# Optimization experiments

Hardware: AMD Instinct MI355X
Metric: run time of the kernel (lower is better)

## Reference

```python
import jax, jax.numpy as jnp
import numpy as np

PATCH_WEIGHT = 0.5  # module init kwarg
B, C, H = 2, 4, 128  # vol dims (H=W=D)
N, P = 128, 32       # num patches total, patch edge (Hp=Wp=Dp)


def setup_inputs() -> dict:
    key = jax.random.key(0)
    k1, k2, k3 = jax.random.split(key, 3)
    patches = jax.random.normal(k1, (N, C, P, P, P), dtype=jnp.float32)
    vol = jax.random.normal(k2, (B, C, H, H, H), dtype=jnp.float32)
    # lower bound in [0, H-P] so the PxPxP slice stays in-bounds; center = lower + P//2
    crop_centers = jax.random.randint(k3, (N, 3), 0, H - P + 1, dtype=jnp.int32) + P // 2
    return {"patches": patches, "vol": vol, "crop_centers": crop_centers}


def reference(patches, vol, crop_centers):
    n, c_dim, p = patches.shape[0], patches.shape[1], patches.shape[2]
    b_dim = vol.shape[0]
    num_patch_per_batch = n // b_dim
    b_idx = jnp.arange(n) // num_patch_per_batch            # [N] batch index per patch
    lo = crop_centers - p // 2                              # [N,3] slice lower bounds
    offs = jnp.arange(p)
    hi = lo[:, 0, None] + offs                              # [N,P]
    wi = lo[:, 1, None] + offs                              # [N,P]
    di = lo[:, 2, None] + offs                              # [N,P]
    c_idx = jnp.arange(c_dim)
    # module: new_vol = vol*(1-pw); w_t is overwritten with ones, so add pw*patch
    new_vol = vol * (1.0 - PATCH_WEIGHT)
    new_vol = new_vol.at[
        b_idx[:, None, None, None, None],
        c_idx[None, :, None, None, None],
        hi[:, None, :, None, None],
        wi[:, None, None, :, None],
        di[:, None, None, None, :],
    ].add(patches * PATCH_WEIGHT)                           # scatter-add handles overlaps
    return new_vol
```

## Files before the change

### kernel.cpp

```cpp
#include <hip/hip_runtime.h>


constexpr int C = 4, H = 128, P = 32;
constexpr int NPB  = 64;
constexpr int CH4  = H * H * H / 4;
constexpr int PCH4 = P * P * P / 4;

__global__ __launch_bounds__(256) void patch_gather_kernel(
        const float4* __restrict__ patches4,
        const int*   __restrict__ centers,
        const float4* __restrict__ vol4,
        float4* __restrict__ out4) {
    __shared__ int s_list[NPB];
    __shared__ int s_n;

    int blk = blockIdx.x;
    int b   = blk >> 11;
    int blo = blk & 2047;
    int tid = threadIdx.x;

    int h  = blo >> 4;
    int w0 = (blo & 15) << 3;

    int d4 = tid & 31;
    int w  = w0 + (tid >> 5);
    int d0 = d4 << 2;

    int base4 = (((b * C) * H + h) * H + w) * 32 + d4;
    float4 v0 = vol4[base4];
    float4 v1 = vol4[base4 + CH4];
    float4 v2 = vol4[base4 + 2 * CH4];
    float4 v3 = vol4[base4 + 3 * CH4];

    if (tid < 64) {
        int lo0 = centers[(b * NPB + tid) * 3 + 0] - 16;
        int lo1 = centers[(b * NPB + tid) * 3 + 1] - 16;
        int lo2 = centers[(b * NPB + tid) * 3 + 2] - 16;
        bool hit = ((unsigned)(h - lo0) < 32u) &&
                   ((unsigned)(w0 - lo1 + 7) < 39u);
        unsigned long long m = __ballot(hit);
        if (hit) {
            int pos = __popcll(m & ((1ull << tid) - 1ull));
            s_list[pos] = (tid << 21) | ((h - lo0) << 14) | (lo1 << 7) | lo2;
        }
        if (tid == 0) s_n = __popcll(m);
    }
    __syncthreads();

    int nh = s_n;
    float4 acc[4] = {};
    const float4* pbat = patches4 + (size_t)b * NPB * C * PCH4;

    int enext = (nh > 0) ? s_list[0] : 0;
    for (int i = 0; i < nh; ++i) {
        int e = enext;
        enext = s_list[(i + 1 < nh) ? i + 1 : i];
        int pn  = e >> 21;
        int hi  = (e >> 14) & 31;
        int lo1 = (e >> 7) & 127;
        int lo2 = e & 127;
        int wi  = w - lo1;
        int k0  = d0 - lo2;
        bool hit = ((unsigned)wi < 32u) && (k0 > -4) && (k0 < 32);

        float4 z = make_float4(0.f, 0.f, 0.f, 0.f);
        float4 a0 = z, a1 = z, a2 = z, a3 = z, b0 = z, b1 = z, b2 = z, b3 = z;
        if (hit) {
            int q = (k0 + 4) >> 2;
            int ka = q - 1, kb = q;
            const float4* pr = pbat + (size_t)pn * C * PCH4 + (hi * 32 + wi) * 8;
            if ((unsigned)ka < 8u) {
                a0 = pr[ka];           a1 = pr[PCH4 + ka];
                a2 = pr[2 * PCH4 + ka]; a3 = pr[3 * PCH4 + ka];
            }
            if ((unsigned)kb < 8u) {
                b0 = pr[kb];           b1 = pr[PCH4 + kb];
                b2 = pr[2 * PCH4 + kb]; b3 = pr[3 * PCH4 + kb];
            }
        }
        int shift = __builtin_amdgcn_readfirstlane(k0 & 3);

#define SH0(c, A, B) acc[c].x += A.x; acc[c].y += A.y; acc[c].z += A.z; acc[c].w += A.w;
#define SH1(c, A, B) acc[c].x += A.y; acc[c].y += A.z; acc[c].z += A.w; acc[c].w += B.x;
#define SH2(c, A, B) acc[c].x += A.z; acc[c].y += A.w; acc[c].z += B.x; acc[c].w += B.y;
#define SH3(c, A, B) acc[c].x += A.w; acc[c].y += B.x; acc[c].z += B.y; acc[c].w += B.z;
        switch (shift) {
        case 0: SH0(0, a0, b0) SH0(1, a1, b1) SH0(2, a2, b2) SH0(3, a3, b3) break;
        case 1: SH1(0, a0, b0) SH1(1, a1, b1) SH1(2, a2, b2) SH1(3, a3, b3) break;
        case 2: SH2(0, a0, b0) SH2(1, a1, b1) SH2(2, a2, b2) SH2(3, a3, b3) break;
        default: SH3(0, a0, b0) SH3(1, a1, b1) SH3(2, a2, b2) SH3(3, a3, b3) break;
        }
    }

    float4 o;
    o.x = (v0.x + acc[0].x) * 0.5f; o.y = (v0.y + acc[0].y) * 0.5f;
    o.z = (v0.z + acc[0].z) * 0.5f; o.w = (v0.w + acc[0].w) * 0.5f;
    out4[base4] = o;
    o.x = (v1.x + acc[1].x) * 0.5f; o.y = (v1.y + acc[1].y) * 0.5f;
    o.z = (v1.z + acc[1].z) * 0.5f; o.w = (v1.w + acc[1].w) * 0.5f;
    out4[base4 + CH4] = o;
    o.x = (v2.x + acc[2].x) * 0.5f; o.y = (v2.y + acc[2].y) * 0.5f;
    o.z = (v2.z + acc[2].z) * 0.5f; o.w = (v2.w + acc[2].w) * 0.5f;
    out4[base4 + 2 * CH4] = o;
    o.x = (v3.x + acc[3].x) * 0.5f; o.y = (v3.y + acc[3].y) * 0.5f;
    o.z = (v3.z + acc[3].z) * 0.5f; o.w = (v3.w + acc[3].w) * 0.5f;
    out4[base4 + 3 * CH4] = o;
}

extern "C" void kernel_launch(void* const* d_in, const int* in_sizes, int n_in,
                              void* d_out, int out_size, void* d_ws, size_t ws_size,
                              hipStream_t stream) {
    const float* patches = (const float*)d_in[0];
    const float* vol     = (const float*)d_in[1];
    const int*   centers = (const int*)d_in[2];
    float* out = (float*)d_out;

    patch_gather_kernel<<<4096, 256, 0, stream>>>(
        (const float4*)patches, centers, (const float4*)vol, (float4*)out);
}
```

Before: 59.12 us.

## Split channels across blocks instead of processing four channels per thread

Each block now handles a single channel, so the grid grows fourfold and each thread loads, accumulates and stores one float4 instead of four. This lowers per-thread register pressure and raises parallelism and occupancy. In exchange, the center list is rebuilt four times as often and the prefetch of the next list entry is dropped.

```diff
diff --git a/kernel.cpp b/kernel.cpp
--- a/kernel.cpp
+++ b/kernel.cpp
@@ -3,7 +3,6 @@
 
 constexpr int C = 4, H = 128, P = 32;
 constexpr int NPB  = 64;
-constexpr int CH4  = H * H * H / 4;
 constexpr int PCH4 = P * P * P / 4;
 
 __global__ __launch_bounds__(256) void patch_gather_kernel(
@@ -15,22 +14,19 @@
     __shared__ int s_n;
 
     int blk = blockIdx.x;
-    int b   = blk >> 11;
-    int blo = blk & 2047;
-    int tid = threadIdx.x;
+    int wgrp = blk & 15;
+    int h    = (blk >> 4) & 127;
+    int c    = (blk >> 11) & 3;
+    int b    = blk >> 13;
+    int tid  = threadIdx.x;
 
-    int h  = blo >> 4;
-    int w0 = (blo & 15) << 3;
-
+    int w0 = wgrp << 3;
     int d4 = tid & 31;
     int w  = w0 + (tid >> 5);
     int d0 = d4 << 2;
 
-    int base4 = (((b * C) * H + h) * H + w) * 32 + d4;
-    float4 v0 = vol4[base4];
-    float4 v1 = vol4[base4 + CH4];
-    float4 v2 = vol4[base4 + 2 * CH4];
-    float4 v3 = vol4[base4 + 3 * CH4];
+    int base4 = (((b * C + c) * H + h) * H + w) * 32 + d4;
+    float4 v = vol4[base4];
 
     if (tid < 64) {
         int lo0 = centers[(b * NPB + tid) * 3 + 0] - 16;
@@ -48,13 +44,11 @@
     __syncthreads();
 
     int nh = s_n;
-    float4 acc[4] = {};
-    const float4* pbat = patches4 + (size_t)b * NPB * C * PCH4;
+    float4 acc = make_float4(0.f, 0.f, 0.f, 0.f);
+    const float4* pbat = patches4 + ((size_t)b * NPB * C + c) * PCH4;
 
-    int enext = (nh > 0) ? s_list[0] : 0;
     for (int i = 0; i < nh; ++i) {
-        int e = enext;
-        enext = s_list[(i + 1 < nh) ? i + 1 : i];
+        int e   = s_list[i];
         int pn  = e >> 21;
         int hi  = (e >> 14) & 31;
         int lo1 = (e >> 7) & 127;
@@ -64,47 +58,33 @@
         bool hit = ((unsigned)wi < 32u) && (k0 > -4) && (k0 < 32);
 
         float4 z = make_float4(0.f, 0.f, 0.f, 0.f);
-        float4 a0 = z, a1 = z, a2 = z, a3 = z, b0 = z, b1 = z, b2 = z, b3 = z;
+        float4 A = z, Bv = z;
         if (hit) {
             int q = (k0 + 4) >> 2;
             int ka = q - 1, kb = q;
             const float4* pr = pbat + (size_t)pn * C * PCH4 + (hi * 32 + wi) * 8;
-            if ((unsigned)ka < 8u) {
-                a0 = pr[ka];           a1 = pr[PCH4 + ka];
-                a2 = pr[2 * PCH4 + ka]; a3 = pr[3 * PCH4 + ka];
-            }
-            if ((unsigned)kb < 8u) {
-                b0 = pr[kb];           b1 = pr[PCH4 + kb];
-                b2 = pr[2 * PCH4 + kb]; b3 = pr[3 * PCH4 + kb];
-            }
+            if ((unsigned)ka < 8u) A  = pr[ka];
+            if ((unsigned)kb < 8u) Bv = pr[kb];
         }
         int shift = __builtin_amdgcn_readfirstlane(k0 & 3);
-
-#define SH0(c, A, B) acc[c].x += A.x; acc[c].y += A.y; acc[c].z += A.z; acc[c].w += A.w;
-#define SH1(c, A, B) acc[c].x += A.y; acc[c].y += A.z; acc[c].z += A.w; acc[c].w += B.x;
-#define SH2(c, A, B) acc[c].x += A.z; acc[c].y += A.w; acc[c].z += B.x; acc[c].w += B.y;
-#define SH3(c, A, B) acc[c].x += A.w; acc[c].y += B.x; acc[c].z += B.y; acc[c].w += B.z;
         switch (shift) {
-        case 0: SH0(0, a0, b0) SH0(1, a1, b1) SH0(2, a2, b2) SH0(3, a3, b3) break;
-        case 1: SH1(0, a0, b0) SH1(1, a1, b1) SH1(2, a2, b2) SH1(3, a3, b3) break;
-        case 2: SH2(0, a0, b0) SH2(1, a1, b1) SH2(2, a2, b2) SH2(3, a3, b3) break;
-        default: SH3(0, a0, b0) SH3(1, a1, b1) SH3(2, a2, b2) SH3(3, a3, b3) break;
+        case 0:
+            acc.x += A.x; acc.y += A.y; acc.z += A.z; acc.w += A.w; break;
+        case 1:
+            acc.x += A.y; acc.y += A.z; acc.z += A.w; acc.w += Bv.x; break;
+        case 2:
+            acc.x += A.z; acc.y += A.w; acc.z += Bv.x; acc.w += Bv.y; break;
+        default:
+            acc.x += A.w; acc.y += Bv.x; acc.z += Bv.y; acc.w += Bv.z; break;
         }
     }
 
     float4 o;
-    o.x = (v0.x + acc[0].x) * 0.5f; o.y = (v0.y + acc[0].y) * 0.5f;
-    o.z = (v0.z + acc[0].z) * 0.5f; o.w = (v0.w + acc[0].w) * 0.5f;
+    o.x = (v.x + acc.x) * 0.5f;
+    o.y = (v.y + acc.y) * 0.5f;
+    o.z = (v.z + acc.z) * 0.5f;
+    o.w = (v.w + acc.w) * 0.5f;
     out4[base4] = o;
-    o.x = (v1.x + acc[1].x) * 0.5f; o.y = (v1.y + acc[1].y) * 0.5f;
-    o.z = (v1.z + acc[1].z) * 0.5f; o.w = (v1.w + acc[1].w) * 0.5f;
-    out4[base4 + CH4] = o;
-    o.x = (v2.x + acc[2].x) * 0.5f; o.y = (v2.y + acc[2].y) * 0.5f;
-    o.z = (v2.z + acc[2].z) * 0.5f; o.w = (v2.w + acc[2].w) * 0.5f;
-    out4[base4 + 2 * CH4] = o;
-    o.x = (v3.x + acc[3].x) * 0.5f; o.y = (v3.y + acc[3].y) * 0.5f;
-    o.z = (v3.z + acc[3].z) * 0.5f; o.w = (v3.w + acc[3].w) * 0.5f;
-    out4[base4 + 3 * CH4] = o;
 }
 
 extern "C" void kernel_launch(void* const* d_in, const int* in_sizes, int n_in,
@@ -115,6 +95,6 @@
     const int*   centers = (const int*)d_in[2];
     float* out = (float*)d_out;
 
-    patch_gather_kernel<<<4096, 256, 0, stream>>>(
+    patch_gather_kernel<<<16384, 256, 0, stream>>>(
         (const float4*)patches, centers, (const float4*)vol, (float4*)out);
 }
```

Result: no change. 59.71 us (+1.0%).
